# Kernel tuning notes

Hardware: AMD Instinct MI355X
Metric: run time of the kernel (lower is better)

Reference implementation:

```python
import jax, jax.numpy as jnp
import numpy as np

DIM = 192
HEADS = 4
EPS_LN = 1e-5
EPS_NORM = 1e-12


def _layernorm(x, w, b):
    # x: [b, c, h, w]; normalize over channel dim (equiv to 'b (h w) c' LN over last axis)
    mu = jnp.mean(x, axis=1, keepdims=True)
    var = jnp.mean((x - mu) ** 2, axis=1, keepdims=True)
    return (x - mu) / jnp.sqrt(var + EPS_LN) * w[None, :, None, None] + b[None, :, None, None]


def _conv1x1(x, w):
    # w: [out_c, in_c]
    return jnp.einsum('bchw,oc->bohw', x, w)


def _dwconv3x3(x, w):
    # w: [c, 1, 3, 3], depthwise (groups = c), padding 1
    return jax.lax.conv_general_dilated(
        x, w, window_strides=(1, 1), padding='SAME',
        feature_group_count=x.shape[1],
        dimension_numbers=('NCHW', 'OIHW', 'NCHW'))


def _l2norm(x):
    # F.normalize(dim=-1): x / max(||x||_2, eps)
    n = jnp.sqrt(jnp.sum(x * x, axis=-1, keepdims=True))
    return x / jnp.maximum(n, EPS_NORM)


def setup_inputs() -> dict:
    key = jax.random.key(0)
    ks = jax.random.split(key, 10)
    b, c, h, w = 8, DIM, 128, 128
    inp = {
        'xx': jax.random.normal(ks[0], (b, c, h, w), jnp.float32),
        'q_in': jax.random.normal(ks[1], (b, c, h, w), jnp.float32),
        'ln_w': jnp.ones((c,), jnp.float32),
        'ln_b': jnp.zeros((c,), jnp.float32),
        'w_q': jax.random.normal(ks[2], (c, c), jnp.float32) * 0.02,
        'w_k': jax.random.normal(ks[3], (c, c), jnp.float32) * 0.02,
        'w_v': jax.random.normal(ks[4], (c, c), jnp.float32) * 0.02,
        'wd_q': jax.random.normal(ks[5], (c, 1, 3, 3), jnp.float32) * 0.1,
        'wd_k': jax.random.normal(ks[6], (c, 1, 3, 3), jnp.float32) * 0.1,
        'wd_v': jax.random.normal(ks[7], (c, 1, 3, 3), jnp.float32) * 0.1,
        'w_proj': jax.random.normal(ks[8], (c, c), jnp.float32) * 0.02,
        'temperature': jnp.ones((HEADS, 1, 1), jnp.float32),
    }
    return inp


def reference(xx, q_in, ln_w, ln_b, w_q, w_k, w_v, wd_q, wd_k, wd_v, w_proj, temperature):
    b, c, h, w = xx.shape
    hw = h * w
    dh = c // HEADS  # per-head channel dim

    x_n = _layernorm(xx, ln_w, ln_b)
    q_n = _layernorm(q_in, ln_w, ln_b)

    q = _dwconv3x3(_conv1x1(q_n, w_q), wd_q)
    k = _dwconv3x3(_conv1x1(x_n, w_k), wd_k)
    v = _dwconv3x3(_conv1x1(x_n, w_v), wd_v)

    # b (head c) h w -> b head c (h w)
    q = q.reshape(b, HEADS, dh, hw)
    k = k.reshape(b, HEADS, dh, hw)
    v = v.reshape(b, HEADS, dh, hw)

    q = _l2norm(q)
    k = _l2norm(k)

    # channel-channel attention: [b, head, dh, dh]
    attn = jnp.einsum('bhcn,bhdn->bhcd', q, k) * temperature[None]
    attn = jax.nn.softmax(attn, axis=-1)

    out = jnp.einsum('bhcd,bhdn->bhcn', attn, v)  # [b, head, dh, hw]
    out = out.reshape(b, c, h, w)
    out = _conv1x1(out, w_proj) + q_in
    return out
```

## Files before the change

### kernel.cpp

```cpp
#include <hip/hip_runtime.h>
#include <hip/hip_bf16.h>
#include <stdint.h>

#define HWSZ 16384
#define CCH 192
#define NB 8
#define NHEAD 4
#define DHEAD 48

typedef unsigned short u16;
typedef __bf16 bf16x8 __attribute__((ext_vector_type(8)));
typedef float f32x4 __attribute__((ext_vector_type(4)));
typedef short s16x8 __attribute__((ext_vector_type(8)));
typedef short s16x4 __attribute__((ext_vector_type(4)));

__device__ __forceinline__ float b2f(u16 h){
  union { unsigned u; float f; } v; v.u = ((unsigned)h) << 16; return v.f;
}
__device__ __forceinline__ u16 f2b(float f){
  union { float f; unsigned u; } v; v.f = f;
  unsigned r = v.u + 0x7fffu + ((v.u >> 16) & 1u);
  return (u16)(r >> 16);
}

__global__ __launch_bounds__(256) void k_wpack(
    const float* __restrict__ wq, const float* __restrict__ wk,
    const float* __restrict__ wv,
    const float* __restrict__ lnw, const float* __restrict__ lnb,
    u16* __restrict__ o, float* __restrict__ ad)
{
  int m = blockIdx.x;
  const float* src = (m == 0) ? wq : (m == 1) ? wk : wv;
  u16* dst = o + (size_t)m * CCH * CCH;
  int t = threadIdx.x;
  if (t < CCH){
    const float* row = src + (size_t)t * CCH;
    float a = 0.f, d = 0.f;
    for (int c = 0; c < CCH; c += 4){
      float4 w = *(const float4*)(row + c);
      float4 g = *(const float4*)(lnw + c);
      float4 bb = *(const float4*)(lnb + c);
      u16 p0 = f2b(w.x * g.x), p1 = f2b(w.y * g.y);
      u16 p2 = f2b(w.z * g.z), p3 = f2b(w.w * g.w);
      a += b2f(p0) + b2f(p1) + b2f(p2) + b2f(p3);
      d += w.x * bb.x + w.y * bb.y + w.z * bb.z + w.w * bb.w;
      s16x4 pk;
      pk[0] = (short)p0; pk[1] = (short)p1; pk[2] = (short)p2; pk[3] = (short)p3;
      *(s16x4*)(dst + (size_t)t * CCH + c) = pk;
    }
    ad[(m * 2 + 0) * CCH + t] = a;
    ad[(m * 2 + 1) * CCH + t] = d;
  }
}

__global__ __launch_bounds__(256, 4) void k_convf(
    const float* __restrict__ xx, const float* __restrict__ q_in,
    const u16* __restrict__ Wb, const float* __restrict__ ad,
    u16* __restrict__ Ok, u16* __restrict__ Ov, u16* __restrict__ Oq)
{
  __shared__ u16 lnT[48 * 264];
  __shared__ float2 redf[4][64];
  __shared__ float2 mures[64];
  int tid = threadIdx.x;
  int b = blockIdx.y, z = blockIdx.z;
  int p0 = blockIdx.x * 64;
  int grp = tid & 7;
  int cs  = tid >> 3;
  int lane = tid & 63, w = tid >> 6;

  const float* xb = (z ? q_in : xx) + (size_t)b * CCH * HWSZ + p0 + grp * 8;

  float4 v[12];
  #pragma unroll
  for (int i = 0; i < 6; ++i){
    v[2 * i]     = *(const float4*)(xb + (size_t)(i * 32 + cs) * HWSZ);
    v[2 * i + 1] = *(const float4*)(xb + (size_t)(i * 32 + cs) * HWSZ + 4);
  }
  float s[8] = {}, ss[8] = {};
  #pragma unroll
  for (int i = 0; i < 6; ++i){
    float e0 = v[2*i].x, e1 = v[2*i].y, e2 = v[2*i].z, e3 = v[2*i].w;
    float e4 = v[2*i+1].x, e5 = v[2*i+1].y, e6 = v[2*i+1].z, e7 = v[2*i+1].w;
    s[0] += e0; ss[0] += e0*e0;  s[1] += e1; ss[1] += e1*e1;
    s[2] += e2; ss[2] += e2*e2;  s[3] += e3; ss[3] += e3*e3;
    s[4] += e4; ss[4] += e4*e4;  s[5] += e5; ss[5] += e5*e5;
    s[6] += e6; ss[6] += e6*e6;  s[7] += e7; ss[7] += e7*e7;
  }
  #pragma unroll
  for (int i = 0; i < 6; ++i){
    s16x8 pk;
    pk[0] = (short)f2b(v[2*i].x);   pk[1] = (short)f2b(v[2*i].y);
    pk[2] = (short)f2b(v[2*i].z);   pk[3] = (short)f2b(v[2*i].w);
    pk[4] = (short)f2b(v[2*i+1].x); pk[5] = (short)f2b(v[2*i+1].y);
    pk[6] = (short)f2b(v[2*i+1].z); pk[7] = (short)f2b(v[2*i+1].w);
    int tile = (cs >> 2) & 1;
    int mr   = ((cs >> 3) << 2) | (cs & 3);
    int ti   = (i * 4 + (grp >> 1)) * 2 + tile;
    *(s16x8*)(&lnT[ti * 264 + mr * 16 + (grp & 1) * 8]) = pk;
  }
  #pragma unroll
  for (int m = 8; m <= 32; m <<= 1){
    #pragma unroll
    for (int j = 0; j < 8; ++j){
      s[j]  += __shfl_xor(s[j],  m);
      ss[j] += __shfl_xor(ss[j], m);
    }
  }
  if (lane < 8){
    #pragma unroll
    for (int j = 0; j < 8; ++j)
      redf[w][lane * 8 + j] = make_float2(s[j], ss[j]);
  }
  __syncthreads();

  if (tid < 64){
    float2 t0 = redf[0][tid], t1 = redf[1][tid];
    float2 t2 = redf[2][tid], t3 = redf[3][tid];
    float s_ = t0.x + t1.x + t2.x + t3.x;
    float q_ = t0.y + t1.y + t2.y + t3.y;
    float mu = s_ * (1.f / CCH);
    float var = q_ * (1.f / CCH) - mu * mu;
    mures[tid] = make_float2(mu, rsqrtf(var + 1e-5f));
  }

  int quad = lane >> 4, r = lane & 15;
  int wm = w * 48;
  int nt = z ? 1 : 2;
  size_t ob = (size_t)b * CCH * HWSZ;
  unsigned lvb0 = (unsigned)(uintptr_t)(&lnT[0]) + 2u * (unsigned)(r + quad * 64);

  for (int t = 0; t < nt; ++t){
    int mi = z ? 0 : (t + 1);
    const u16* A0 = Wb + (size_t)mi * CCH * CCH + (size_t)wm * CCH;
    const float* aA = ad + (mi * 2 + 0) * CCH;
    const float* dA = ad + (mi * 2 + 1) * CCH;
    u16* O = z ? Oq : (t ? Ov : Ok);
    f32x4 acc[3][4] = {};
    bf16x8 aC[3], aN[3];
    #pragma unroll
    for (int i = 0; i < 3; ++i)
      aC[i] = *(const bf16x8*)(A0 + (size_t)(i * 16 + r) * CCH + quad * 8);
    #pragma unroll
    for (int kb = 0; kb < 6; ++kb){
      s16x4 lo[4], hi[4];
      #pragma unroll
      for (int j = 0; j < 4; ++j){
        unsigned a = lvb0 + (unsigned)(kb * 4224 + j * 1056);
        asm volatile("ds_read_b64_tr_b16 %0, %1" : "=&v"(lo[j]) : "v"(a));
        asm volatile("ds_read_b64_tr_b16 %0, %1 offset:528" : "=&v"(hi[j]) : "v"(a));
      }
      if (kb < 5){
        #pragma unroll
        for (int i = 0; i < 3; ++i)
          aN[i] = *(const bf16x8*)(A0 + (size_t)(i * 16 + r) * CCH + (kb + 1) * 32 + quad * 8);
      }
      asm volatile("s_waitcnt lgkmcnt(0)" ::: "memory");
      __builtin_amdgcn_sched_barrier(0);
      #pragma unroll
      for (int j = 0; j < 4; ++j){
        union { s16x8 s; bf16x8 b; } u;
        u.s = __builtin_shufflevector(lo[j], hi[j], 0, 1, 2, 3, 4, 5, 6, 7);
        #pragma unroll
        for (int i = 0; i < 3; ++i)
          acc[i][j] = __builtin_amdgcn_mfma_f32_16x16x32_bf16(aC[i], u.b, acc[i][j], 0, 0, 0);
      }
      #pragma unroll
      for (int i = 0; i < 3; ++i) aC[i] = aN[i];
    }
    if (t == 0) __syncthreads();
    #pragma unroll
    for (int j = 0; j < 4; ++j){
      int px = j * 16 + r;
      float2 mr_ = mures[px];
      #pragma unroll
      for (int i = 0; i < 3; ++i){
        #pragma unroll
        for (int rg = 0; rg < 4; ++rg){
          int o = wm + i * 16 + quad * 4 + rg;
          float val = mr_.y * (acc[i][j][rg] - mr_.x * aA[o]) + dA[o];
          O[ob + (size_t)o * HWSZ + p0 + px] = f2b(val);
        }
      }
    }
  }
}

__global__ __launch_bounds__(256) void k_dw3(
    const float* __restrict__ wq, const float* __restrict__ wk,
    const float* __restrict__ wv,
    u16* __restrict__ bq, u16* __restrict__ bk, u16* __restrict__ bv,
    float* __restrict__ ssq_q, float* __restrict__ ssq_k)
{
  int tid = threadIdx.x;
  int bc  = blockIdx.x;
  int z   = blockIdx.y;
  int c   = bc % CCH;
  const float* wd = (z == 0) ? wq : (z == 1) ? wk : wv;
  u16* buf = (z == 0) ? bq : (z == 1) ? bk : bv;
  float w[9];
  #pragma unroll
  for (int t = 0; t < 9; ++t) w[t] = wd[c * 9 + t];
  u16* p = buf + (size_t)bc * HWSZ;

  int xseg = tid & 15, ygrp = tid >> 4;
  int x0 = xseg * 8, y0 = ygrp * 8;

  s16x8 zz = {0,0,0,0,0,0,0,0};
  s16x8 raw[10];
  #pragma unroll
  for (int rr = 0; rr < 10; ++rr){
    int yy = y0 - 1 + rr;
    raw[rr] = (yy >= 0 && yy < 128) ? *(const s16x8*)(p + yy * 128 + x0) : zz;
  }
  __syncthreads();

  float cf[10][8];
  float lf[10], rgt[10];
  #pragma unroll
  for (int rr = 0; rr < 10; ++rr){
    #pragma unroll
    for (int j = 0; j < 8; ++j) cf[rr][j] = b2f((u16)raw[rr][j]);
    float l  = __shfl_up(cf[rr][7], 1);
    float rr_ = __shfl_down(cf[rr][0], 1);
    lf[rr]  = (xseg > 0)  ? l   : 0.f;
    rgt[rr] = (xseg < 15) ? rr_ : 0.f;
  }

  float ss = 0.f;
  #pragma unroll
  for (int k = 0; k < 8; ++k){
    float acc[8] = {0.f,0.f,0.f,0.f,0.f,0.f,0.f,0.f};
    #pragma unroll
    for (int dy = 0; dy < 3; ++dy){
      int rr = k + dy;
      float wl = w[dy * 3], wc = w[dy * 3 + 1], wr = w[dy * 3 + 2];
      acc[0] += wl * lf[rr] + wc * cf[rr][0] + wr * cf[rr][1];
      #pragma unroll
      for (int j = 1; j < 7; ++j)
        acc[j] += wl * cf[rr][j - 1] + wc * cf[rr][j] + wr * cf[rr][j + 1];
      acc[7] += wl * cf[rr][6] + wc * cf[rr][7] + wr * rgt[rr];
    }
    s16x8 pk;
    #pragma unroll
    for (int j = 0; j < 8; ++j){
      pk[j] = (short)f2b(acc[j]);
      ss += acc[j] * acc[j];
    }
    *(s16x8*)(p + (y0 + k) * 128 + x0) = pk;
  }

  if (z < 2){
    #pragma unroll
    for (int m = 32; m > 0; m >>= 1) ss += __shfl_xor(ss, m);
    if ((tid & 63) == 0) atomicAdd(&((z == 0) ? ssq_q : ssq_k)[bc], ss);
  }
}

__global__ void k_gram(const u16* __restrict__ q, const u16* __restrict__ k,
                       float* __restrict__ G)
{
  __shared__ float gs[4 * 48 * 49];
  int tid = threadIdx.x;
  int chunk = blockIdx.x;
  int h = blockIdx.y, b = blockIdx.z;
  int lane = tid & 63, w = tid >> 6;
  int quad = lane >> 4, r = lane & 15;
  int nb = chunk * 1024 + w * 256;
  const u16* qb = q + ((size_t)b * CCH + h * DHEAD) * HWSZ;
  const u16* kb = k + ((size_t)b * CCH + h * DHEAD) * HWSZ;
  f32x4 acc[3][3] = {};
  for (int s = 0; s < 8; ++s){
    int kk = nb + s * 32 + quad * 8;
    bf16x8 af[3], bfr[3];
    #pragma unroll
    for (int i = 0; i < 3; ++i){
      af[i]  = *(const bf16x8*)(qb + (size_t)(i * 16 + r) * HWSZ + kk);
      bfr[i] = *(const bf16x8*)(kb + (size_t)(i * 16 + r) * HWSZ + kk);
    }
    #pragma unroll
    for (int i = 0; i < 3; ++i)
      #pragma unroll
      for (int j = 0; j < 3; ++j)
        acc[i][j] = __builtin_amdgcn_mfma_f32_16x16x32_bf16(af[i], bfr[j], acc[i][j], 0, 0, 0);
  }
  float* gw = gs + w * (48 * 49);
  #pragma unroll
  for (int i = 0; i < 3; ++i)
    #pragma unroll
    for (int j = 0; j < 3; ++j)
      #pragma unroll
      for (int rg = 0; rg < 4; ++rg){
        int row = i * 16 + quad * 4 + rg;
        int col = j * 16 + r;
        gw[row * 49 + col] = acc[i][j][rg];
      }
  __syncthreads();
  float* gb = G + (size_t)(b * NHEAD + h) * (DHEAD * DHEAD);
  #pragma unroll
  for (int t = 0; t < 9; ++t){
    int e = t * 256 + tid;
    int row = e / 48, col = e - row * 48;
    int o = row * 49 + col;
    float s = gs[o] + gs[48 * 49 + o] + gs[2 * 48 * 49 + o] + gs[3 * 48 * 49 + o];
    atomicAdd(&gb[e], s);
  }
}

__global__ __launch_bounds__(256) void k_mk(
    const float* __restrict__ G, const float* __restrict__ ssq_q,
    const float* __restrict__ ssq_k, const float* __restrict__ temp,
    const float* __restrict__ wp, u16* __restrict__ Mout)
{
  __shared__ u16 Pt[48 * 72];
  __shared__ u16 wA[192 * 72];
  __shared__ float rks[48];
  int tid = threadIdx.x;
  int h = blockIdx.x, b = blockIdx.y;
  {
    s16x8 z = {};
    #pragma unroll
    for (int i = 0; i < 2; ++i){
      int idx = (i * 256 + tid) * 8;
      if (idx < 48 * 72) *(s16x8*)(&Pt[idx]) = z;
    }
    #pragma unroll
    for (int i = 0; i < 7; ++i){
      int idx = (i * 256 + tid) * 8;
      if (idx < 192 * 72) *(s16x8*)(&wA[idx]) = z;
    }
  }
  if (tid < DHEAD)
    rks[tid] = 1.f / fmaxf(sqrtf(ssq_k[b * CCH + h * DHEAD + tid]), 1e-12f);
  __syncthreads();
  if (tid < DHEAD){
    float rq = temp[h] / fmaxf(sqrtf(ssq_q[b * CCH + h * DHEAD + tid]), 1e-12f);
    const float* gr = G + (size_t)(b * NHEAD + h) * (DHEAD * DHEAD) + tid * DHEAD;
    float a[DHEAD];
    float mx = -1e30f;
    #pragma unroll
    for (int d = 0; d < DHEAD; ++d){
      a[d] = gr[d] * rq * rks[d];
      mx = fmaxf(mx, a[d]);
    }
    float sum = 0.f;
    #pragma unroll
    for (int d = 0; d < DHEAD; ++d){ a[d] = __expf(a[d] - mx); sum += a[d]; }
    float inv = 1.f / sum;
    #pragma unroll
    for (int d = 0; d < DHEAD; ++d) Pt[d * 72 + tid] = f2b(a[d] * inv);
  }
  {
    const float* wb = wp + h * DHEAD;
    #pragma unroll
    for (int i = 0; i < 9; ++i){
      int e = (i * 256 + tid) * 4;
      int row = e / DHEAD, col = e - row * DHEAD;
      float4 v = *(const float4*)(wb + (size_t)row * CCH + col);
      s16x4 pk;
      pk[0] = (short)f2b(v.x); pk[1] = (short)f2b(v.y);
      pk[2] = (short)f2b(v.z); pk[3] = (short)f2b(v.w);
      *(s16x4*)(&wA[row * 72 + col]) = pk;
    }
  }
  __syncthreads();
  int lane = tid & 63, wid = tid >> 6;
  int quad = lane >> 4, r = lane & 15;
  int wm = wid * 48;
  f32x4 acc[3][3] = {};
  #pragma unroll
  for (int ks = 0; ks < 2; ++ks){
    int k0 = ks * 32;
    bf16x8 af[3], bf[3];
    #pragma unroll
    for (int i = 0; i < 3; ++i)
      af[i] = *(const bf16x8*)(&wA[(wm + i * 16 + r) * 72 + k0 + quad * 8]);
    #pragma unroll
    for (int j = 0; j < 3; ++j)
      bf[j] = *(const bf16x8*)(&Pt[(j * 16 + r) * 72 + k0 + quad * 8]);
    #pragma unroll
    for (int i = 0; i < 3; ++i)
      #pragma unroll
      for (int j = 0; j < 3; ++j)
        acc[i][j] = __builtin_amdgcn_mfma_f32_16x16x32_bf16(af[i], bf[j], acc[i][j], 0, 0, 0);
  }
  u16* mb = Mout + (size_t)b * (CCH * CCH) + h * DHEAD;
  #pragma unroll
  for (int i = 0; i < 3; ++i)
    #pragma unroll
    for (int j = 0; j < 3; ++j)
      #pragma unroll
      for (int rg = 0; rg < 4; ++rg){
        int o = wm + i * 16 + quad * 4 + rg;
        int d = j * 16 + r;
        mb[(size_t)o * CCH + d] = f2b(acc[i][j][rg]);
      }
}

__global__ __launch_bounds__(256) void k_gemmv(
    const u16* __restrict__ M, const u16* __restrict__ V,
    float* __restrict__ Out, const float* __restrict__ resid)
{
  __shared__ u16 lA[64 * 200];
  __shared__ u16 lV[96 * 264];
  int tid = threadIdx.x;
  int n0 = blockIdx.x * 128;
  int m0 = blockIdx.y * 64;
  int b  = blockIdx.z;
  {
    const u16* ap = M + (size_t)b * (CCH * CCH) + m0 * CCH;
    #pragma unroll
    for (int i = 0; i < 6; ++i){
      int off = (i * 256 + tid) * 8;
      int row = off / CCH, col = off - row * CCH;
      *(int4*)(&lA[row * 200 + col]) = *(const int4*)(ap + off);
    }
  }
  {
    const u16* vp = V + (size_t)b * CCH * HWSZ + n0;
    #pragma unroll
    for (int i = 0; i < 12; ++i){
      int e = i * 256 + tid;
      int c = e >> 4, ns = (e & 15) * 8;
      int4 v = *(const int4*)(vp + (size_t)c * HWSZ + ns);
      int kb = c >> 5, kr = c & 31;
      int tile = (kr >> 2) & 1;
      int mr = ((kr >> 3) << 2) | (kr & 3);
      int ti = (kb * 8 + (ns >> 4)) * 2 + tile;
      *(int4*)(&lV[ti * 264 + mr * 16 + (ns & 15)]) = v;
    }
  }
  __syncthreads();
  int lane = tid & 63, wid = tid >> 6;
  int quad = lane >> 4, r = lane & 15;
  int wm = (wid >> 1) * 32, wn = (wid & 1) * 64;
  unsigned lvb = (unsigned)(uintptr_t)(&lV[0]) + 2u * (unsigned)(r + quad * 64)
               + (unsigned)((wn >> 4) * 2) * 528u;
  f32x4 acc[2][4] = {};
  #pragma unroll
  for (int kb = 0; kb < 6; ++kb){
    int k0 = kb * 32;
    s16x4 lo[4], hi[4];
    #pragma unroll
    for (int j = 0; j < 4; ++j){
      unsigned a = lvb + (unsigned)kb * 8448u + (unsigned)j * 1056u;
      asm volatile("ds_read_b64_tr_b16 %0, %1" : "=&v"(lo[j]) : "v"(a));
      asm volatile("ds_read_b64_tr_b16 %0, %1 offset:528" : "=&v"(hi[j]) : "v"(a));
    }
    bf16x8 af[2];
    #pragma unroll
    for (int i = 0; i < 2; ++i)
      af[i] = *(const bf16x8*)(&lA[(wm + i * 16 + r) * 200 + k0 + quad * 8]);
    asm volatile("s_waitcnt lgkmcnt(0)" ::: "memory");
    __builtin_amdgcn_sched_barrier(0);
    #pragma unroll
    for (int j = 0; j < 4; ++j){
      union { s16x8 s; bf16x8 b; } u;
      u.s = __builtin_shufflevector(lo[j], hi[j], 0, 1, 2, 3, 4, 5, 6, 7);
      #pragma unroll
      for (int i = 0; i < 2; ++i)
        acc[i][j] = __builtin_amdgcn_mfma_f32_16x16x32_bf16(af[i], u.b, acc[i][j], 0, 0, 0);
    }
  }
  size_t obase = (size_t)b * CCH * HWSZ;
  #pragma unroll
  for (int i = 0; i < 2; ++i){
    #pragma unroll
    for (int rg = 0; rg < 4; ++rg){
      int o = m0 + wm + i * 16 + quad * 4 + rg;
      size_t rowb = obase + (size_t)o * HWSZ;
      #pragma unroll
      for (int j = 0; j < 4; ++j){
        int n = n0 + wn + j * 16 + r;
        Out[rowb + n] = acc[i][j][rg] + resid[rowb + n];
      }
    }
  }
}

extern "C" void kernel_launch(void* const* d_in, const int* in_sizes, int n_in,
                              void* d_out, int out_size, void* d_ws, size_t ws_size,
                              hipStream_t stream)
{
  const float* xx     = (const float*)d_in[0];
  const float* q_in   = (const float*)d_in[1];
  const float* ln_w   = (const float*)d_in[2];
  const float* ln_b   = (const float*)d_in[3];
  const float* w_q    = (const float*)d_in[4];
  const float* w_k    = (const float*)d_in[5];
  const float* w_v    = (const float*)d_in[6];
  const float* wd_q   = (const float*)d_in[7];
  const float* wd_k   = (const float*)d_in[8];
  const float* wd_v   = (const float*)d_in[9];
  const float* w_proj = (const float*)d_in[10];
  const float* temp   = (const float*)d_in[11];

  const size_t SZ = (size_t)NB * CCH * HWSZ;
  u16* B1 = (u16*)d_ws;
  u16* B2 = B1 + SZ;
  u16* B3 = B2 + SZ;
  float* G     = (float*)(B3 + SZ);
  float* ssq_q = G + 32 * DHEAD * DHEAD;
  float* ssq_k = ssq_q + NB * CCH;
  u16* Mb      = (u16*)(ssq_k + NB * CCH);
  u16* Wb      = Mb + (size_t)NB * CCH * CCH;
  float* Ad    = (float*)(Wb + 3 * CCH * CCH);

  hipMemsetAsync(G, 0, (size_t)(32 * DHEAD * DHEAD + 2 * NB * CCH) * sizeof(float), stream);

  k_wpack<<<3, 256, 0, stream>>>(w_q, w_k, w_v, ln_w, ln_b, Wb, Ad);
  k_convf<<<dim3(256, NB, 2), 256, 0, stream>>>(
      xx, q_in, Wb, Ad, B2, B1, B3);
  k_dw3<<<dim3(NB * CCH, 3), 256, 0, stream>>>(wd_q, wd_k, wd_v,
                                               B3, B2, B1, ssq_q, ssq_k);
  k_gram<<<dim3(16, NHEAD, NB), 256, 0, stream>>>(B3, B2, G);
  k_mk<<<dim3(NHEAD, NB), 256, 0, stream>>>(G, ssq_q, ssq_k, temp, w_proj, Mb);
  k_gemmv<<<dim3(128, 3, NB), 256, 0, stream>>>(Mb, B1, (float*)d_out, q_in);
}
```

Baseline: 482.6 us.

## Widen fused LN+conv1x1 tiles to 256 pixels with 512-thread blocks

The fused layernorm plus 1x1 conv kernel now processes 256 pixels per block with 512 threads instead of 64 pixels with 256 threads, so each staged activation tile in LDS is reused across more MFMA work. For the xx input, the K and V projections are split across wave groups instead of run sequentially. Swapping the MFMA operand order transposes the accumulator layout, which allows packed 4-wide bf16 stores along the pixel dimension instead of scalar 2-byte stores. Normalization constants are hoisted into registers. The cost is much more LDS per block (about 100KB), which lowers occupancy, and fewer blocks in the grid.

```diff
diff --git a/kernel.cpp b/kernel.cpp
--- a/kernel.cpp
+++ b/kernel.cpp
@@ -53,88 +53,99 @@
   }
 }
 
-__global__ __launch_bounds__(256, 4) void k_convf(
+__global__ __launch_bounds__(512, 2) void k_convf2(
     const float* __restrict__ xx, const float* __restrict__ q_in,
     const u16* __restrict__ Wb, const float* __restrict__ ad,
     u16* __restrict__ Ok, u16* __restrict__ Ov, u16* __restrict__ Oq)
 {
-  __shared__ u16 lnT[48 * 264];
-  __shared__ float2 redf[4][64];
-  __shared__ float2 mures[64];
+  __shared__ u16 lnT[6 * 16 * 2 * 264];
+  __shared__ float2 redf[8][256];
+  __shared__ float mu_s[256];
+  __shared__ float rs_s[256];
   int tid = threadIdx.x;
   int b = blockIdx.y, z = blockIdx.z;
-  int p0 = blockIdx.x * 64;
-  int grp = tid & 7;
-  int cs  = tid >> 3;
+  int p0 = blockIdx.x * 256;
   int lane = tid & 63, w = tid >> 6;
+  int grp = tid & 31;
+  int cr  = tid >> 5;
 
   const float* xb = (z ? q_in : xx) + (size_t)b * CCH * HWSZ + p0 + grp * 8;
 
-  float4 v[12];
-  #pragma unroll
-  for (int i = 0; i < 6; ++i){
-    v[2 * i]     = *(const float4*)(xb + (size_t)(i * 32 + cs) * HWSZ);
-    v[2 * i + 1] = *(const float4*)(xb + (size_t)(i * 32 + cs) * HWSZ + 4);
-  }
   float s[8] = {}, ss[8] = {};
   #pragma unroll
-  for (int i = 0; i < 6; ++i){
-    float e0 = v[2*i].x, e1 = v[2*i].y, e2 = v[2*i].z, e3 = v[2*i].w;
-    float e4 = v[2*i+1].x, e5 = v[2*i+1].y, e6 = v[2*i+1].z, e7 = v[2*i+1].w;
-    s[0] += e0; ss[0] += e0*e0;  s[1] += e1; ss[1] += e1*e1;
-    s[2] += e2; ss[2] += e2*e2;  s[3] += e3; ss[3] += e3*e3;
-    s[4] += e4; ss[4] += e4*e4;  s[5] += e5; ss[5] += e5*e5;
-    s[6] += e6; ss[6] += e6*e6;  s[7] += e7; ss[7] += e7*e7;
-  }
-  #pragma unroll
-  for (int i = 0; i < 6; ++i){
-    s16x8 pk;
-    pk[0] = (short)f2b(v[2*i].x);   pk[1] = (short)f2b(v[2*i].y);
-    pk[2] = (short)f2b(v[2*i].z);   pk[3] = (short)f2b(v[2*i].w);
-    pk[4] = (short)f2b(v[2*i+1].x); pk[5] = (short)f2b(v[2*i+1].y);
-    pk[6] = (short)f2b(v[2*i+1].z); pk[7] = (short)f2b(v[2*i+1].w);
-    int tile = (cs >> 2) & 1;
-    int mr   = ((cs >> 3) << 2) | (cs & 3);
-    int ti   = (i * 4 + (grp >> 1)) * 2 + tile;
-    *(s16x8*)(&lnT[ti * 264 + mr * 16 + (grp & 1) * 8]) = pk;
-  }
-  #pragma unroll
-  for (int m = 8; m <= 32; m <<= 1){
-    #pragma unroll
-    for (int j = 0; j < 8; ++j){
-      s[j]  += __shfl_xor(s[j],  m);
-      ss[j] += __shfl_xor(ss[j], m);
-    }
-  }
-  if (lane < 8){
+  for (int pass = 0; pass < 2; ++pass){
+    float4 v[12];
+    #pragma unroll
+    for (int ii = 0; ii < 6; ++ii){
+      int c = (pass * 6 + ii) * 16 + cr;
+      v[2*ii]   = *(const float4*)(xb + (size_t)c * HWSZ);
+      v[2*ii+1] = *(const float4*)(xb + (size_t)c * HWSZ + 4);
+    }
+    #pragma unroll
+    for (int ii = 0; ii < 6; ++ii){
+      int c = (pass * 6 + ii) * 16 + cr;
+      float e0 = v[2*ii].x,   e1 = v[2*ii].y,   e2 = v[2*ii].z,   e3 = v[2*ii].w;
+      float e4 = v[2*ii+1].x, e5 = v[2*ii+1].y, e6 = v[2*ii+1].z, e7 = v[2*ii+1].w;
+      s[0]+=e0; ss[0]+=e0*e0; s[1]+=e1; ss[1]+=e1*e1;
+      s[2]+=e2; ss[2]+=e2*e2; s[3]+=e3; ss[3]+=e3*e3;
+      s[4]+=e4; ss[4]+=e4*e4; s[5]+=e5; ss[5]+=e5*e5;
+      s[6]+=e6; ss[6]+=e6*e6; s[7]+=e7; ss[7]+=e7*e7;
+      s16x8 pk;
+      pk[0]=(short)f2b(e0); pk[1]=(short)f2b(e1); pk[2]=(short)f2b(e2); pk[3]=(short)f2b(e3);
+      pk[4]=(short)f2b(e4); pk[5]=(short)f2b(e5); pk[6]=(short)f2b(e6); pk[7]=(short)f2b(e7);
+      int kb = c >> 5, kr = c & 31;
+      int tile = (kr >> 2) & 1;
+      int mr   = ((kr >> 3) << 2) | (kr & 3);
+      int ti   = (kb * 16 + (grp >> 1)) * 2 + tile;
+      *(s16x8*)(&lnT[ti * 264 + mr * 16 + (grp & 1) * 8]) = pk;
+    }
+  }
+  #pragma unroll
+  for (int j = 0; j < 8; ++j){
+    s[j]  += __shfl_xor(s[j],  32);
+    ss[j] += __shfl_xor(ss[j], 32);
+  }
+  if (lane < 32){
     #pragma unroll
     for (int j = 0; j < 8; ++j)
-      redf[w][lane * 8 + j] = make_float2(s[j], ss[j]);
-  }
-  __syncthreads();
-
-  if (tid < 64){
-    float2 t0 = redf[0][tid], t1 = redf[1][tid];
-    float2 t2 = redf[2][tid], t3 = redf[3][tid];
-    float s_ = t0.x + t1.x + t2.x + t3.x;
-    float q_ = t0.y + t1.y + t2.y + t3.y;
-    float mu = s_ * (1.f / CCH);
-    float var = q_ * (1.f / CCH) - mu * mu;
-    mures[tid] = make_float2(mu, rsqrtf(var + 1e-5f));
-  }
+      redf[w][grp * 8 + j] = make_float2(s[j], ss[j]);
+  }
+  __syncthreads();
+  if (tid < 256){
+    float sa = 0.f, qa = 0.f;
+    #pragma unroll
+    for (int ww = 0; ww < 8; ++ww){
+      float2 t = redf[ww][tid];
+      sa += t.x; qa += t.y;
+    }
+    float mu = sa * (1.f / CCH);
+    float var = qa * (1.f / CCH) - mu * mu;
+    mu_s[tid] = mu;
+    rs_s[tid] = rsqrtf(var + 1e-5f);
+  }
+  __syncthreads();
 
   int quad = lane >> 4, r = lane & 15;
-  int wm = w * 48;
-  int nt = z ? 1 : 2;
+  int wm = (w & 3) * 48;
+  int mi, nh0, nhn;
+  if (z == 0){ mi = (w >> 2) + 1; nh0 = 0; nhn = 4; }
+  else       { mi = 0; nh0 = (w >> 2) * 2; nhn = 2; }
+  const u16* A0 = Wb + (size_t)mi * CCH * CCH + (size_t)wm * CCH;
+  const float* aA = ad + (mi * 2 + 0) * CCH;
+  const float* dA = ad + (mi * 2 + 1) * CCH;
+  u16* O = z ? Oq : ((w >> 2) ? Ov : Ok);
   size_t ob = (size_t)b * CCH * HWSZ;
   unsigned lvb0 = (unsigned)(uintptr_t)(&lnT[0]) + 2u * (unsigned)(r + quad * 64);
 
-  for (int t = 0; t < nt; ++t){
-    int mi = z ? 0 : (t + 1);
-    const u16* A0 = Wb + (size_t)mi * CCH * CCH + (size_t)wm * CCH;
-    const float* aA = ad + (mi * 2 + 0) * CCH;
-    const float* dA = ad + (mi * 2 + 1) * CCH;
-    u16* O = z ? Oq : (t ? Ov : Ok);
+  float a_o[3], d_o[3];
+  #pragma unroll
+  for (int i = 0; i < 3; ++i){
+    a_o[i] = aA[wm + i * 16 + r];
+    d_o[i] = dA[wm + i * 16 + r];
+  }
+
+  for (int hh = 0; hh < nhn; ++hh){
+    int nh = nh0 + hh;
     f32x4 acc[3][4] = {};
     bf16x8 aC[3], aN[3];
     #pragma unroll
@@ -145,7 +156,7 @@
       s16x4 lo[4], hi[4];
       #pragma unroll
       for (int j = 0; j < 4; ++j){
-        unsigned a = lvb0 + (unsigned)(kb * 4224 + j * 1056);
+        unsigned a = lvb0 + (unsigned)(kb * 16896 + (nh * 4 + j) * 1056);
         asm volatile("ds_read_b64_tr_b16 %0, %1" : "=&v"(lo[j]) : "v"(a));
         asm volatile("ds_read_b64_tr_b16 %0, %1 offset:528" : "=&v"(hi[j]) : "v"(a));
       }
@@ -162,24 +173,26 @@
         u.s = __builtin_shufflevector(lo[j], hi[j], 0, 1, 2, 3, 4, 5, 6, 7);
         #pragma unroll
         for (int i = 0; i < 3; ++i)
-          acc[i][j] = __builtin_amdgcn_mfma_f32_16x16x32_bf16(aC[i], u.b, acc[i][j], 0, 0, 0);
+          acc[i][j] = __builtin_amdgcn_mfma_f32_16x16x32_bf16(u.b, aC[i], acc[i][j], 0, 0, 0);
       }
       #pragma unroll
       for (int i = 0; i < 3; ++i) aC[i] = aN[i];
     }
-    if (t == 0) __syncthreads();
     #pragma unroll
     for (int j = 0; j < 4; ++j){
-      int px = j * 16 + r;
-      float2 mr_ = mures[px];
+      int pxb = nh * 64 + j * 16 + quad * 4;
+      f32x4 mu4 = *(const f32x4*)(&mu_s[pxb]);
+      f32x4 rs4 = *(const f32x4*)(&rs_s[pxb]);
       #pragma unroll
       for (int i = 0; i < 3; ++i){
+        s16x4 pk;
         #pragma unroll
         for (int rg = 0; rg < 4; ++rg){
-          int o = wm + i * 16 + quad * 4 + rg;
-          float val = mr_.y * (acc[i][j][rg] - mr_.x * aA[o]) + dA[o];
-          O[ob + (size_t)o * HWSZ + p0 + px] = f2b(val);
+          float val = rs4[rg] * (acc[i][j][rg] - mu4[rg] * a_o[i]) + d_o[i];
+          pk[rg] = (short)f2b(val);
         }
+        int o = wm + i * 16 + r;
+        *(s16x4*)(&O[ob + (size_t)o * HWSZ + p0 + pxb]) = pk;
       }
     }
   }
@@ -508,7 +521,7 @@
   hipMemsetAsync(G, 0, (size_t)(32 * DHEAD * DHEAD + 2 * NB * CCH) * sizeof(float), stream);
 
   k_wpack<<<3, 256, 0, stream>>>(w_q, w_k, w_v, ln_w, ln_b, Wb, Ad);
-  k_convf<<<dim3(256, NB, 2), 256, 0, stream>>>(
+  k_convf2<<<dim3(64, NB, 2), 512, 0, stream>>>(
       xx, q_in, Wb, Ad, B2, B1, B3);
   k_dw3<<<dim3(NB * CCH, 3), 256, 0, stream>>>(wd_q, wd_k, wd_v,
                                                B3, B2, B1, ssq_q, ssq_k);
```

Result: faster. 445.7 us (-7.6%).
